# Optimization experiments

Hardware: AMD Instinct MI355X
Metric: run time of the kernel (lower is better)

## Reference

```python
import jax, jax.numpy as jnp
import numpy as np

D_MODEL = 1024
NUM_HEADS = 16
THETA = 10000.0


def _rope(x, pos):
    # x: [B, H, S, d_k], pos: [B, S] int
    d = x.shape[-1]
    half = d // 2
    inv_freq = THETA ** (-(jnp.arange(half, dtype=jnp.float32) * 2.0) / d)  # [half]
    ang = pos.astype(jnp.float32)[..., None] * inv_freq                     # [B, S, half]
    cos = jnp.cos(ang)[:, None, :, :]  # [B, 1, S, half]
    sin = jnp.sin(ang)[:, None, :, :]
    x1 = x[..., 0::2]
    x2 = x[..., 1::2]
    r1 = x1 * cos - x2 * sin
    r2 = x1 * sin + x2 * cos
    return jnp.stack([r1, r2], axis=-1).reshape(x.shape)


def setup_inputs() -> dict:
    key = jax.random.key(0)
    ks = jax.random.split(key, 5)
    B, S, D = 2, 2048, D_MODEL
    scale = 1.0 / np.sqrt(D)
    x = jax.random.normal(ks[0], (B, S, D), dtype=jnp.float32)
    token_positions = jnp.broadcast_to(jnp.arange(S, dtype=jnp.int32), (B, S))
    Wq = jax.random.normal(ks[1], (D, D), dtype=jnp.float32) * scale
    Wk = jax.random.normal(ks[2], (D, D), dtype=jnp.float32) * scale
    Wv = jax.random.normal(ks[3], (D, D), dtype=jnp.float32) * scale
    Wo = jax.random.normal(ks[4], (D, D), dtype=jnp.float32) * scale
    return {"x": x, "token_positions": token_positions, "Wq": Wq, "Wk": Wk, "Wv": Wv, "Wo": Wo}


def reference(x, token_positions, Wq, Wk, Wv, Wo):
    B, S, D = x.shape
    H = NUM_HEADS
    dk = D // H
    # Linear: y = x @ W.T (torch nn.Linear convention, no bias)
    q = jnp.einsum('bsd,od->bso', x, Wq).reshape(B, S, H, dk).transpose(0, 2, 1, 3)
    k = jnp.einsum('bsd,od->bso', x, Wk).reshape(B, S, H, dk).transpose(0, 2, 1, 3)
    v = jnp.einsum('bsd,od->bso', x, Wv).reshape(B, S, H, dk).transpose(0, 2, 1, 3)
    q = _rope(q, token_positions)
    k = _rope(k, token_positions)
    scores = jnp.einsum('bhqd,bhkd->bhqk', q, k) / jnp.sqrt(jnp.float32(dk))
    causal = jnp.tril(jnp.ones((S, S), dtype=bool))
    scores = jnp.where(causal, scores, jnp.finfo(scores.dtype).min)
    attn = jax.nn.softmax(scores, axis=-1)
    out = jnp.einsum('bhqk,bhkd->bhqd', attn, v)  # [B, H, S, dk]
    out = out.transpose(0, 2, 1, 3).reshape(B, S, D)
    return jnp.einsum('bsd,od->bso', out, Wo)
```

## Files before the change

### kernel.cpp

```cpp
#include <hip/hip_runtime.h>
#include <stdint.h>

#define S_LEN 2048
#define DMODEL 1024
#define NHEAD 16
#define DK 64
#define BATCH 2

typedef __attribute__((ext_vector_type(8))) short bf16x8;
typedef __attribute__((ext_vector_type(4))) float f32x4;

__device__ __forceinline__ unsigned short f2bf(float f) {
  union { float f; unsigned u; } x; x.f = f;
  unsigned u = x.u;
  return (unsigned short)((u + 0x7fffu + ((u >> 16) & 1u)) >> 16);
}

__device__ __forceinline__ uint cvt_pk_bf16(float a, float b) {
  uint r;
  asm("v_cvt_pk_bf16_f32 %0, %1, %2" : "=v"(r) : "v"(a), "v"(b));
  return r;
}

__device__ __forceinline__ void gload_lds16(const void* g, void* l) {
  __builtin_amdgcn_global_load_lds(
      (const __attribute__((address_space(1))) unsigned int*)g,
      (__attribute__((address_space(3))) unsigned int*)l, 16, 0, 0);
}

#define QSCALE 0.18033688011112042f

__global__ __launch_bounds__(256) void cast_inputs(
    const float4* __restrict__ x,
    const float4* __restrict__ wq, const float4* __restrict__ wk,
    const float4* __restrict__ wv, const float4* __restrict__ wo,
    ushort4* __restrict__ xb, ushort4* __restrict__ wqkvb, ushort4* __restrict__ wob,
    const int* __restrict__ pos, float2* __restrict__ rope)
{
  int i = blockIdx.x * 256 + threadIdx.x;
  const int NCAST = (1 << 21);
  if (i < NCAST) {
    float4 v; ushort4* dst;
    if (i < (1 << 20)) {
      v = x[i]; dst = xb + i;
    } else {
      int j = i - (1 << 20);
      int wsel = j >> 18;
      int o = j & ((1 << 18) - 1);
      const float4* src = (wsel == 0) ? wq : (wsel == 1) ? wk : (wsel == 2) ? wv : wo;
      v = src[o];
      dst = (wsel < 3) ? (wqkvb + ((size_t)wsel << 18) + o) : (wob + o);
    }
    ushort4 r;
    r.x = f2bf(v.x); r.y = f2bf(v.y); r.z = f2bf(v.z); r.w = f2bf(v.w);
    *dst = r;
  } else {
    int idx = i - NCAST;
    if (idx < 4096 * 32) {
      int ps = idx >> 5;
      int fi = idx & 31;
      float p = (float)pos[ps];
      float freq = exp2f(-(float)fi * 0.41524101186092096f);
      float ang = p * freq;
      rope[idx] = make_float2(cosf(ang), sinf(ang));
    }
  }
}

template<int EPI>
__global__ __launch_bounds__(256) void gemm_bt(
    const ushort* __restrict__ A, const ushort* __restrict__ Bw,
    const float2* __restrict__ rope,
    ushort* __restrict__ Qb, ushort* __restrict__ Kb, ushort* __restrict__ Vg,
    float* __restrict__ Out)
{
  constexpr int Kdim = 1024;
  __shared__ ushort At[128 * 64];
  __shared__ ushort Bt[128 * 64];
  const int bm = blockIdx.x & 31;
  const int bn = blockIdx.x >> 5;
  const int tid = threadIdx.x;
  const int w = tid >> 6, lane = tid & 63;
  const int wr = w >> 1, wc = w & 1;
  const int lrow = lane >> 3;
  const int lch = lane & 7;

  f32x4 acc[4][4];
#pragma unroll
  for (int i = 0; i < 4; ++i)
#pragma unroll
    for (int j = 0; j < 4; ++j) acc[i][j] = (f32x4){0.f, 0.f, 0.f, 0.f};

  const size_t abase = (size_t)(bm * 128) * Kdim;
  const size_t bbase = (size_t)(bn * 128) * Kdim;

  for (int kt = 0; kt < Kdim / 64; ++kt) {
#pragma unroll
    for (int inst = 0; inst < 4; ++inst) {
      int r = w * 32 + inst * 8 + lrow;
      int gc = lch ^ (r & 7);
      gload_lds16(A + abase + (size_t)r * Kdim + kt * 64 + gc * 8,
                  &At[(w * 32 + inst * 8) * 64]);
      gload_lds16(Bw + bbase + (size_t)r * Kdim + kt * 64 + gc * 8,
                  &Bt[(w * 32 + inst * 8) * 64]);
    }
    __syncthreads();
    __builtin_amdgcn_s_setprio(1);
#pragma unroll
    for (int kk = 0; kk < 2; ++kk) {
      bf16x8 af[4], bfv[4];
      int ch = kk * 4 + (lane >> 4);
#pragma unroll
      for (int fm = 0; fm < 4; ++fm) {
        int row = wr * 64 + fm * 16 + (lane & 15);
        af[fm] = *(const bf16x8*)&At[row * 64 + ((ch ^ (row & 7)) << 3)];
      }
#pragma unroll
      for (int fn = 0; fn < 4; ++fn) {
        int row = wc * 64 + fn * 16 + (lane & 15);
        bfv[fn] = *(const bf16x8*)&Bt[row * 64 + ((ch ^ (row & 7)) << 3)];
      }
#pragma unroll
      for (int fm = 0; fm < 4; ++fm)
#pragma unroll
        for (int fn = 0; fn < 4; ++fn)
          acc[fm][fn] = __builtin_amdgcn_mfma_f32_16x16x32_bf16(
              af[fm], bfv[fn], acc[fm][fn], 0, 0, 0);
    }
    __builtin_amdgcn_s_setprio(0);
    __syncthreads();
  }

  if constexpr (EPI == 0) {
    const int sel = bn >> 3;
    if (sel == 2) {
#pragma unroll
      for (int fn = 0; fn < 4; ++fn) {
        int gn = bn * 128 + wc * 64 + fn * 16 + (lane & 15);
        int col = gn & 1023;
        int h = col >> 6, d = col & 63;
#pragma unroll
        for (int fm = 0; fm < 4; ++fm) {
          int gm0 = bm * 128 + wr * 64 + fm * 16 + ((lane >> 4) << 2);
          int b = gm0 >> 11, s0 = gm0 & 2047;
          uint lo = cvt_pk_bf16(acc[fm][fn][0], acc[fm][fn][1]);
          uint hi2 = cvt_pk_bf16(acc[fm][fn][2], acc[fm][fn][3]);
          uint2 val; val.x = lo; val.y = hi2;
          *(uint2*)(Vg + ((size_t)((b * NHEAD + h) * DK + d) * S_LEN) + s0) = val;
        }
      }
    } else {
      ushort* dst0 = (sel == 0) ? Qb : Kb;
#pragma unroll
      for (int fn = 0; fn < 4; ++fn) {
        int gn = bn * 128 + wc * 64 + fn * 16 + (lane & 15);
        int col = gn & 1023;
        int h = col >> 6, d = col & 63;
#pragma unroll
        for (int fm = 0; fm < 4; ++fm) {
          int gm0 = bm * 128 + wr * 64 + fm * 16 + ((lane >> 4) << 2);
#pragma unroll
          for (int j = 0; j < 4; ++j) {
            int gm = gm0 + j;
            float v = acc[fm][fn][j];
            float p = __shfl_xor(v, 1);
            float2 cs = rope[gm * 32 + (d >> 1)];
            float r = (d & 1) ? (v * cs.x + p * cs.y) : (v * cs.x - p * cs.y);
            if (sel == 0) r *= QSCALE;
            int b = gm >> 11, s = gm & 2047;
            dst0[((size_t)(b * NHEAD + h) * S_LEN + s) * DK + d] = f2bf(r);
          }
        }
      }
    }
  } else {
#pragma unroll
    for (int fn = 0; fn < 4; ++fn) {
      int gn = bn * 128 + wc * 64 + fn * 16 + (lane & 15);
#pragma unroll
      for (int fm = 0; fm < 4; ++fm) {
        int gm0 = bm * 128 + wr * 64 + fm * 16 + ((lane >> 4) << 2);
#pragma unroll
        for (int j = 0; j < 4; ++j)
          Out[(size_t)(gm0 + j) * 1024 + gn] = acc[fm][fn][j];
      }
    }
  }
}

__global__ __launch_bounds__(256) void attn_kernel(
    const ushort* __restrict__ Qb, const ushort* __restrict__ Kb,
    const ushort* __restrict__ Vg, ushort* __restrict__ Ob)
{
  __shared__ ushort Kt[2][64 * 64];
  __shared__ ushort Vt[2][64 * 64];
  __shared__ ushort Pt[4][16 * 64];
  const int tid = threadIdx.x;
  const int w = tid >> 6, lane = tid & 63;
  const int g = lane >> 4, q = lane & 15;
  const int bid = blockIdx.x;
  const int swz = (bid & 7) * 64 + (bid >> 3);
  const int bh = swz >> 4, pair = swz & 15;
  const size_t kqbase = (size_t)bh * (S_LEN * DK);
  const size_t vbase  = (size_t)bh * (DK * S_LEN);
  const int b = bh >> 4, h = bh & 15;
  ushort* Pw = Pt[w];
  uint* Pw32 = (uint*)Pw;

  for (int t2 = 0; t2 < 2; ++t2) {
    const int qt = t2 ? (31 - pair) : pair;
    const int qrow0 = qt * 64 + w * 16;

    bf16x8 qf[2];
    {
      const ushort* qp = Qb + kqbase + (size_t)(qrow0 + q) * DK + g * 8;
      qf[0] = *(const bf16x8*)qp;
      qf[1] = *(const bf16x8*)(qp + 32);
    }
    f32x4 oacc[4];
#pragma unroll
    for (int dt = 0; dt < 4; ++dt) oacc[dt] = (f32x4){0.f, 0.f, 0.f, 0.f};
    float m_r = -INFINITY, l_r = 0.f;

#pragma unroll
    for (int pass = 0; pass < 2; ++pass) {
      int r0 = pass * 32 + w * 8;
      int r = r0 + (lane >> 3);
      int gc = (lane & 7) ^ (r & 7);
      gload_lds16(Kb + kqbase + (size_t)r * DK + gc * 8, &Kt[0][r0 * 64]);
      gload_lds16(Vg + vbase + (size_t)r * S_LEN + gc * 8, &Vt[0][r0 * 64]);
    }
    __syncthreads();

    int cur = 0;
    for (int kt = 0; kt <= qt; ++kt) {
      if (kt < qt) {
        int nxt = cur ^ 1, ktn = kt + 1;
#pragma unroll
        for (int pass = 0; pass < 2; ++pass) {
          int r0 = pass * 32 + w * 8;
          int r = r0 + (lane >> 3);
          int gc = (lane & 7) ^ (r & 7);
          gload_lds16(Kb + kqbase + (size_t)(ktn * 64 + r) * DK + gc * 8,
                      &Kt[nxt][r0 * 64]);
          gload_lds16(Vg + vbase + (size_t)r * S_LEN + ktn * 64 + gc * 8,
                      &Vt[nxt][r0 * 64]);
        }
      }

      f32x4 sacc[4];
#pragma unroll
      for (int ct = 0; ct < 4; ++ct) sacc[ct] = (f32x4){0.f, 0.f, 0.f, 0.f};
      __builtin_amdgcn_s_setprio(1);
#pragma unroll
      for (int kk = 0; kk < 2; ++kk) {
        int ch = kk * 4 + g;
#pragma unroll
        for (int ct = 0; ct < 4; ++ct) {
          int row = ct * 16 + q;
          bf16x8 kf = *(const bf16x8*)&Kt[cur][row * 64 + ((ch ^ (row & 7)) << 3)];
          sacc[ct] = __builtin_amdgcn_mfma_f32_16x16x32_bf16(kf, qf[kk], sacc[ct], 0, 0, 0);
        }
      }
      __builtin_amdgcn_s_setprio(0);

      if (kt == qt) {
        int qa = qrow0 + q;
#pragma unroll
        for (int ct = 0; ct < 4; ++ct) {
#pragma unroll
          for (int j = 0; j < 4; ++j) {
            int kv = qt * 64 + ct * 16 + g * 4 + j;
            if (kv > qa) sacc[ct][j] = -INFINITY;
          }
        }
      }

      float mx = sacc[0][0];
#pragma unroll
      for (int ct = 0; ct < 4; ++ct)
#pragma unroll
        for (int j = 0; j < 4; ++j) mx = fmaxf(mx, sacc[ct][j]);
      mx = fmaxf(mx, __shfl_xor(mx, 16));
      mx = fmaxf(mx, __shfl_xor(mx, 32));
      if (mx > m_r + 8.0f) {
        float sc = exp2f(m_r - mx);
        m_r = mx;
        l_r *= sc;
#pragma unroll
        for (int dt = 0; dt < 4; ++dt)
#pragma unroll
          for (int j = 0; j < 4; ++j) oacc[dt][j] *= sc;
      }
      float p[4][4];
      float rs = 0.f;
#pragma unroll
      for (int ct = 0; ct < 4; ++ct)
#pragma unroll
        for (int j = 0; j < 4; ++j) {
          float e = exp2f(sacc[ct][j] - m_r);
          p[ct][j] = e; rs += e;
        }
      rs += __shfl_xor(rs, 16);
      rs += __shfl_xor(rs, 32);
      l_r += rs;

#pragma unroll
      for (int ct = 0; ct < 4; ++ct)
#pragma unroll
        for (int i = 0; i < 2; ++i) {
          uint u = cvt_pk_bf16(p[ct][2 * i], p[ct][2 * i + 1]);
          int idx = 8 * ct + 2 * g + i;
          Pw32[q * 32 + (((idx >> 2) ^ (q & 7)) << 2) + (idx & 3)] = u;
        }
      __builtin_amdgcn_s_setprio(1);
#pragma unroll
      for (int kk = 0; kk < 2; ++kk) {
        int ch = kk * 4 + g;
        bf16x8 pb = *(const bf16x8*)&Pw[q * 64 + ((ch ^ (q & 7)) << 3)];
#pragma unroll
        for (int dt = 0; dt < 4; ++dt) {
          int vr = dt * 16 + q;
          bf16x8 vf = *(const bf16x8*)&Vt[cur][vr * 64 + ((ch ^ (vr & 7)) << 3)];
          oacc[dt] = __builtin_amdgcn_mfma_f32_16x16x32_bf16(vf, pb, oacc[dt], 0, 0, 0);
        }
      }
      __builtin_amdgcn_s_setprio(0);
      __syncthreads();
      cur ^= 1;
    }

    float inv = 1.0f / l_r;
#pragma unroll
    for (int dt = 0; dt < 4; ++dt)
#pragma unroll
      for (int i = 0; i < 2; ++i) {
        uint u = cvt_pk_bf16(oacc[dt][2 * i] * inv, oacc[dt][2 * i + 1] * inv);
        int idx = dt * 8 + 2 * g + i;
        Pw32[q * 32 + (((idx >> 2) ^ (q & 7)) << 2) + (idx & 3)] = u;
      }
#pragma unroll
    for (int pass = 0; pass < 2; ++pass) {
      int qr = pass * 8 + (lane >> 3), c = lane & 7;
      bf16x8 vv = *(const bf16x8*)&Pw[qr * 64 + ((c ^ (qr & 7)) << 3)];
      *(bf16x8*)(Ob + ((size_t)(b * S_LEN) + qrow0 + qr) * DMODEL + h * DK + c * 8) = vv;
    }
  }
}

extern "C" void kernel_launch(void* const* d_in, const int* in_sizes, int n_in,
                              void* d_out, int out_size, void* d_ws, size_t ws_size,
                              hipStream_t stream) {
  const float* x  = (const float*)d_in[0];
  const int* pos  = (const int*)d_in[1];
  const float* wq = (const float*)d_in[2];
  const float* wk = (const float*)d_in[3];
  const float* wv = (const float*)d_in[4];
  const float* wo = (const float*)d_in[5];
  float* out = (float*)d_out;

  char* ws = (char*)d_ws;
  ushort* xb    = (ushort*)(ws);
  ushort* wqkvb = (ushort*)(ws + (size_t)( 8u << 20));
  ushort* wob   = (ushort*)(ws + (size_t)(14u << 20));
  float2* rope  = (float2*)(ws + (size_t)(16u << 20));
  ushort* Qb    = (ushort*)(ws + (size_t)(17u << 20));
  ushort* Kb    = (ushort*)(ws + (size_t)(25u << 20));
  ushort* Vg    = (ushort*)(ws + (size_t)(33u << 20));
  ushort* Ob    = (ushort*)(ws + (size_t)(41u << 20));

  cast_inputs<<<8704, 256, 0, stream>>>((const float4*)x, (const float4*)wq,
      (const float4*)wk, (const float4*)wv, (const float4*)wo,
      (ushort4*)xb, (ushort4*)wqkvb, (ushort4*)wob, pos, rope);
  gemm_bt<0><<<32 * 24, 256, 0, stream>>>(xb, wqkvb, rope, Qb, Kb, Vg, nullptr);
  attn_kernel<<<512, 256, 0, stream>>>(Qb, Kb, Vg, Ob);
  gemm_bt<1><<<32 * 8, 256, 0, stream>>>(Ob, wob, rope, nullptr, nullptr, nullptr, out);
}
```

Measured before the change: 124.9 us.

## Split attention q-tile pairs across waves and use 64-row tiles for output GEMM

The attention kernel no longer walks its two paired query tiles one after the other. Each block now handles half of both paired tiles at once, with two waves on the late tile and two on the early tile, and all four share one K/V stream up to the longer tile's length. This doubles the grid to 1024 blocks and removes the serial second pass. The output projection moves to a dedicated kernel with 64x128 tiles, giving 512 blocks instead of 256 to better fill the CUs. The cost is that the early-tile waves sit idle on iterations past their causal limit, and the smaller GEMM tile reuses its loaded data less.

```diff
diff --git a/kernel.cpp b/kernel.cpp
--- a/kernel.cpp
+++ b/kernel.cpp
@@ -67,12 +67,10 @@
   }
 }
 
-template<int EPI>
-__global__ __launch_bounds__(256) void gemm_bt(
+__global__ __launch_bounds__(256) void gemm_qkv(
     const ushort* __restrict__ A, const ushort* __restrict__ Bw,
     const float2* __restrict__ rope,
-    ushort* __restrict__ Qb, ushort* __restrict__ Kb, ushort* __restrict__ Vg,
-    float* __restrict__ Out)
+    ushort* __restrict__ Qb, ushort* __restrict__ Kb, ushort* __restrict__ Vg)
 {
   constexpr int Kdim = 1024;
   __shared__ ushort At[128 * 64];
@@ -131,59 +129,124 @@
     __syncthreads();
   }
 
-  if constexpr (EPI == 0) {
-    const int sel = bn >> 3;
-    if (sel == 2) {
-#pragma unroll
-      for (int fn = 0; fn < 4; ++fn) {
-        int gn = bn * 128 + wc * 64 + fn * 16 + (lane & 15);
-        int col = gn & 1023;
-        int h = col >> 6, d = col & 63;
-#pragma unroll
-        for (int fm = 0; fm < 4; ++fm) {
-          int gm0 = bm * 128 + wr * 64 + fm * 16 + ((lane >> 4) << 2);
-          int b = gm0 >> 11, s0 = gm0 & 2047;
-          uint lo = cvt_pk_bf16(acc[fm][fn][0], acc[fm][fn][1]);
-          uint hi2 = cvt_pk_bf16(acc[fm][fn][2], acc[fm][fn][3]);
-          uint2 val; val.x = lo; val.y = hi2;
-          *(uint2*)(Vg + ((size_t)((b * NHEAD + h) * DK + d) * S_LEN) + s0) = val;
-        }
-      }
-    } else {
-      ushort* dst0 = (sel == 0) ? Qb : Kb;
-#pragma unroll
-      for (int fn = 0; fn < 4; ++fn) {
-        int gn = bn * 128 + wc * 64 + fn * 16 + (lane & 15);
-        int col = gn & 1023;
-        int h = col >> 6, d = col & 63;
-#pragma unroll
-        for (int fm = 0; fm < 4; ++fm) {
-          int gm0 = bm * 128 + wr * 64 + fm * 16 + ((lane >> 4) << 2);
-#pragma unroll
-          for (int j = 0; j < 4; ++j) {
-            int gm = gm0 + j;
-            float v = acc[fm][fn][j];
-            float p = __shfl_xor(v, 1);
-            float2 cs = rope[gm * 32 + (d >> 1)];
-            float r = (d & 1) ? (v * cs.x + p * cs.y) : (v * cs.x - p * cs.y);
-            if (sel == 0) r *= QSCALE;
-            int b = gm >> 11, s = gm & 2047;
-            dst0[((size_t)(b * NHEAD + h) * S_LEN + s) * DK + d] = f2bf(r);
-          }
-        }
-      }
-    }
-  } else {
+  const int sel = bn >> 3;
+  if (sel == 2) {
 #pragma unroll
     for (int fn = 0; fn < 4; ++fn) {
       int gn = bn * 128 + wc * 64 + fn * 16 + (lane & 15);
+      int col = gn & 1023;
+      int h = col >> 6, d = col & 63;
 #pragma unroll
       for (int fm = 0; fm < 4; ++fm) {
         int gm0 = bm * 128 + wr * 64 + fm * 16 + ((lane >> 4) << 2);
-#pragma unroll
-        for (int j = 0; j < 4; ++j)
-          Out[(size_t)(gm0 + j) * 1024 + gn] = acc[fm][fn][j];
-      }
+        int b = gm0 >> 11, s0 = gm0 & 2047;
+        uint lo = cvt_pk_bf16(acc[fm][fn][0], acc[fm][fn][1]);
+        uint hi2 = cvt_pk_bf16(acc[fm][fn][2], acc[fm][fn][3]);
+        uint2 val; val.x = lo; val.y = hi2;
+        *(uint2*)(Vg + ((size_t)((b * NHEAD + h) * DK + d) * S_LEN) + s0) = val;
+      }
+    }
+  } else {
+    ushort* dst0 = (sel == 0) ? Qb : Kb;
+#pragma unroll
+    for (int fn = 0; fn < 4; ++fn) {
+      int gn = bn * 128 + wc * 64 + fn * 16 + (lane & 15);
+      int col = gn & 1023;
+      int h = col >> 6, d = col & 63;
+#pragma unroll
+      for (int fm = 0; fm < 4; ++fm) {
+        int gm0 = bm * 128 + wr * 64 + fm * 16 + ((lane >> 4) << 2);
+#pragma unroll
+        for (int j = 0; j < 4; ++j) {
+          int gm = gm0 + j;
+          float v = acc[fm][fn][j];
+          float p = __shfl_xor(v, 1);
+          float2 cs = rope[gm * 32 + (d >> 1)];
+          float r = (d & 1) ? (v * cs.x + p * cs.y) : (v * cs.x - p * cs.y);
+          if (sel == 0) r *= QSCALE;
+          int b = gm >> 11, s = gm & 2047;
+          dst0[((size_t)(b * NHEAD + h) * S_LEN + s) * DK + d] = f2bf(r);
+        }
+      }
+    }
+  }
+}
+
+__global__ __launch_bounds__(256) void gemm_out64(
+    const ushort* __restrict__ A, const ushort* __restrict__ Bw,
+    float* __restrict__ Out)
+{
+  constexpr int Kdim = 1024;
+  __shared__ ushort At[64 * 64];
+  __shared__ ushort Bt[128 * 64];
+  const int bm = blockIdx.x & 63;
+  const int bn = blockIdx.x >> 6;
+  const int tid = threadIdx.x;
+  const int w = tid >> 6, lane = tid & 63;
+  const int wr = w >> 1, wc = w & 1;
+  const int lrow = lane >> 3;
+  const int lch = lane & 7;
+
+  f32x4 acc[2][4];
+#pragma unroll
+  for (int i = 0; i < 2; ++i)
+#pragma unroll
+    for (int j = 0; j < 4; ++j) acc[i][j] = (f32x4){0.f, 0.f, 0.f, 0.f};
+
+  const size_t abase = (size_t)(bm * 64) * Kdim;
+  const size_t bbase = (size_t)(bn * 128) * Kdim;
+
+  for (int kt = 0; kt < Kdim / 64; ++kt) {
+#pragma unroll
+    for (int inst = 0; inst < 2; ++inst) {
+      int r = inst * 32 + w * 8 + lrow;
+      int gc = lch ^ (r & 7);
+      gload_lds16(A + abase + (size_t)r * Kdim + kt * 64 + gc * 8,
+                  &At[(inst * 32 + w * 8) * 64]);
+    }
+#pragma unroll
+    for (int inst = 0; inst < 4; ++inst) {
+      int r = inst * 32 + w * 8 + lrow;
+      int gc = lch ^ (r & 7);
+      gload_lds16(Bw + bbase + (size_t)r * Kdim + kt * 64 + gc * 8,
+                  &Bt[(inst * 32 + w * 8) * 64]);
+    }
+    __syncthreads();
+    __builtin_amdgcn_s_setprio(1);
+#pragma unroll
+    for (int kk = 0; kk < 2; ++kk) {
+      bf16x8 af[2], bfv[4];
+      int ch = kk * 4 + (lane >> 4);
+#pragma unroll
+      for (int fm = 0; fm < 2; ++fm) {
+        int row = wr * 32 + fm * 16 + (lane & 15);
+        af[fm] = *(const bf16x8*)&At[row * 64 + ((ch ^ (row & 7)) << 3)];
+      }
+#pragma unroll
+      for (int fn = 0; fn < 4; ++fn) {
+        int row = wc * 64 + fn * 16 + (lane & 15);
+        bfv[fn] = *(const bf16x8*)&Bt[row * 64 + ((ch ^ (row & 7)) << 3)];
+      }
+#pragma unroll
+      for (int fm = 0; fm < 2; ++fm)
+#pragma unroll
+        for (int fn = 0; fn < 4; ++fn)
+          acc[fm][fn] = __builtin_amdgcn_mfma_f32_16x16x32_bf16(
+              af[fm], bfv[fn], acc[fm][fn], 0, 0, 0);
+    }
+    __builtin_amdgcn_s_setprio(0);
+    __syncthreads();
+  }
+
+#pragma unroll
+  for (int fn = 0; fn < 4; ++fn) {
+    int gn = bn * 128 + wc * 64 + fn * 16 + (lane & 15);
+#pragma unroll
+    for (int fm = 0; fm < 2; ++fm) {
+      int gm0 = bm * 64 + wr * 32 + fm * 16 + ((lane >> 4) << 2);
+#pragma unroll
+      for (int j = 0; j < 4; ++j)
+        Out[(size_t)(gm0 + j) * 1024 + gn] = acc[fm][fn][j];
     }
   }
 }
@@ -198,56 +261,53 @@
   const int tid = threadIdx.x;
   const int w = tid >> 6, lane = tid & 63;
   const int g = lane >> 4, q = lane & 15;
+  const int ww = w & 1;
   const int bid = blockIdx.x;
-  const int swz = (bid & 7) * 64 + (bid >> 3);
-  const int bh = swz >> 4, pair = swz & 15;
+  const int swz = (bid & 7) * 128 + (bid >> 3);
+  const int bh = swz >> 5;
+  const int pair = (swz >> 1) & 15;
+  const int half = swz & 1;
   const size_t kqbase = (size_t)bh * (S_LEN * DK);
   const size_t vbase  = (size_t)bh * (DK * S_LEN);
   const int b = bh >> 4, h = bh & 15;
+  const int qtw = (w < 2) ? (31 - pair) : pair;
+  const int ktmax = 31 - pair;
+  const int qrow0 = qtw * 64 + half * 32 + ww * 16;
   ushort* Pw = Pt[w];
   uint* Pw32 = (uint*)Pw;
 
-  for (int t2 = 0; t2 < 2; ++t2) {
-    const int qt = t2 ? (31 - pair) : pair;
-    const int qrow0 = qt * 64 + w * 16;
-
-    bf16x8 qf[2];
-    {
-      const ushort* qp = Qb + kqbase + (size_t)(qrow0 + q) * DK + g * 8;
-      qf[0] = *(const bf16x8*)qp;
-      qf[1] = *(const bf16x8*)(qp + 32);
-    }
-    f32x4 oacc[4];
-#pragma unroll
-    for (int dt = 0; dt < 4; ++dt) oacc[dt] = (f32x4){0.f, 0.f, 0.f, 0.f};
-    float m_r = -INFINITY, l_r = 0.f;
-
-#pragma unroll
-    for (int pass = 0; pass < 2; ++pass) {
-      int r0 = pass * 32 + w * 8;
-      int r = r0 + (lane >> 3);
-      int gc = (lane & 7) ^ (r & 7);
-      gload_lds16(Kb + kqbase + (size_t)r * DK + gc * 8, &Kt[0][r0 * 64]);
-      gload_lds16(Vg + vbase + (size_t)r * S_LEN + gc * 8, &Vt[0][r0 * 64]);
-    }
-    __syncthreads();
-
-    int cur = 0;
-    for (int kt = 0; kt <= qt; ++kt) {
-      if (kt < qt) {
-        int nxt = cur ^ 1, ktn = kt + 1;
-#pragma unroll
-        for (int pass = 0; pass < 2; ++pass) {
-          int r0 = pass * 32 + w * 8;
-          int r = r0 + (lane >> 3);
-          int gc = (lane & 7) ^ (r & 7);
-          gload_lds16(Kb + kqbase + (size_t)(ktn * 64 + r) * DK + gc * 8,
-                      &Kt[nxt][r0 * 64]);
-          gload_lds16(Vg + vbase + (size_t)r * S_LEN + ktn * 64 + gc * 8,
-                      &Vt[nxt][r0 * 64]);
-        }
-      }
-
+  bf16x8 qf[2];
+  {
+    const ushort* qp = Qb + kqbase + (size_t)(qrow0 + q) * DK + g * 8;
+    qf[0] = *(const bf16x8*)qp;
+    qf[1] = *(const bf16x8*)(qp + 32);
+  }
+  f32x4 oacc[4];
+#pragma unroll
+  for (int dt = 0; dt < 4; ++dt) oacc[dt] = (f32x4){0.f, 0.f, 0.f, 0.f};
+  float m_r = -INFINITY, l_r = 0.f;
+
+#define STAGE(buf_, kt_)                                                     \
+  do {                                                                       \
+    _Pragma("unroll") for (int pass = 0; pass < 2; ++pass) {                 \
+      int r0 = pass * 32 + w * 8;                                            \
+      int r = r0 + (lane >> 3);                                              \
+      int gc = (lane & 7) ^ (r & 7);                                         \
+      gload_lds16(Kb + kqbase + (size_t)((kt_) * 64 + r) * DK + gc * 8,      \
+                  &Kt[buf_][r0 * 64]);                                       \
+      gload_lds16(Vg + vbase + (size_t)r * S_LEN + (kt_) * 64 + gc * 8,      \
+                  &Vt[buf_][r0 * 64]);                                       \
+    }                                                                        \
+  } while (0)
+
+  STAGE(0, 0);
+  __syncthreads();
+
+  int cur = 0;
+  for (int kt = 0; kt <= ktmax; ++kt) {
+    if (kt < ktmax) STAGE(cur ^ 1, kt + 1);
+
+    if (kt <= qtw) {
       f32x4 sacc[4];
 #pragma unroll
       for (int ct = 0; ct < 4; ++ct) sacc[ct] = (f32x4){0.f, 0.f, 0.f, 0.f};
@@ -264,13 +324,13 @@
       }
       __builtin_amdgcn_s_setprio(0);
 
-      if (kt == qt) {
+      if (kt == qtw) {
         int qa = qrow0 + q;
 #pragma unroll
         for (int ct = 0; ct < 4; ++ct) {
 #pragma unroll
           for (int j = 0; j < 4; ++j) {
-            int kv = qt * 64 + ct * 16 + g * 4 + j;
+            int kv = qtw * 64 + ct * 16 + g * 4 + j;
             if (kv > qa) sacc[ct][j] = -INFINITY;
           }
         }
@@ -326,26 +386,28 @@
         }
       }
       __builtin_amdgcn_s_setprio(0);
-      __syncthreads();
-      cur ^= 1;
-    }
-
-    float inv = 1.0f / l_r;
-#pragma unroll
-    for (int dt = 0; dt < 4; ++dt)
-#pragma unroll
-      for (int i = 0; i < 2; ++i) {
-        uint u = cvt_pk_bf16(oacc[dt][2 * i] * inv, oacc[dt][2 * i + 1] * inv);
-        int idx = dt * 8 + 2 * g + i;
-        Pw32[q * 32 + (((idx >> 2) ^ (q & 7)) << 2) + (idx & 3)] = u;
-      }
-#pragma unroll
-    for (int pass = 0; pass < 2; ++pass) {
-      int qr = pass * 8 + (lane >> 3), c = lane & 7;
-      bf16x8 vv = *(const bf16x8*)&Pw[qr * 64 + ((c ^ (qr & 7)) << 3)];
-      *(bf16x8*)(Ob + ((size_t)(b * S_LEN) + qrow0 + qr) * DMODEL + h * DK + c * 8) = vv;
-    }
-  }
+    }
+
+    __syncthreads();
+    cur ^= 1;
+  }
+
+  float inv = 1.0f / l_r;
+#pragma unroll
+  for (int dt = 0; dt < 4; ++dt)
+#pragma unroll
+    for (int i = 0; i < 2; ++i) {
+      uint u = cvt_pk_bf16(oacc[dt][2 * i] * inv, oacc[dt][2 * i + 1] * inv);
+      int idx = dt * 8 + 2 * g + i;
+      Pw32[q * 32 + (((idx >> 2) ^ (q & 7)) << 2) + (idx & 3)] = u;
+    }
+#pragma unroll
+  for (int pass = 0; pass < 2; ++pass) {
+    int qr = pass * 8 + (lane >> 3), c = lane & 7;
+    bf16x8 vv = *(const bf16x8*)&Pw[qr * 64 + ((c ^ (qr & 7)) << 3)];
+    *(bf16x8*)(Ob + ((size_t)(b * S_LEN) + qrow0 + qr) * DMODEL + h * DK + c * 8) = vv;
+  }
+#undef STAGE
 }
 
 extern "C" void kernel_launch(void* const* d_in, const int* in_sizes, int n_in,
@@ -372,7 +434,7 @@
   cast_inputs<<<8704, 256, 0, stream>>>((const float4*)x, (const float4*)wq,
       (const float4*)wk, (const float4*)wv, (const float4*)wo,
       (ushort4*)xb, (ushort4*)wqkvb, (ushort4*)wob, pos, rope);
-  gemm_bt<0><<<32 * 24, 256, 0, stream>>>(xb, wqkvb, rope, Qb, Kb, Vg, nullptr);
-  attn_kernel<<<512, 256, 0, stream>>>(Qb, Kb, Vg, Ob);
-  gemm_bt<1><<<32 * 8, 256, 0, stream>>>(Ob, wob, rope, nullptr, nullptr, nullptr, out);
-}
+  gemm_qkv<<<32 * 24, 256, 0, stream>>>(xb, wqkvb, rope, Qb, Kb, Vg);
+  attn_kernel<<<1024, 256, 0, stream>>>(Qb, Kb, Vg, Ob);
+  gemm_out64<<<512, 256, 0, stream>>>(Ob, wob, out);
+}
```

After: 127.3 us. About the same (+1.9%).
